# Kernel optimization log

Hardware: AMD Instinct MI355X
Metric: run time of the kernel (lower is better)

Reference implementation:

```python
import jax, jax.numpy as jnp
import numpy as np

B, E, T = 2, 512, 2048
H = 8
LOCAL_SIZE = 128
NEG_INF = -1e9


def setup_inputs() -> dict:
    key = jax.random.key(0)
    ks = jax.random.split(key, 5)
    return {
        "x": jax.random.normal(ks[0], (B, E, T), dtype=jnp.float32),
        "in_proj_w": jax.random.normal(ks[1], (3 * E, E), dtype=jnp.float32) * (E ** -0.5),
        "in_proj_b": jax.random.normal(ks[2], (3 * E,), dtype=jnp.float32) * 0.02,
        "out_w": jax.random.normal(ks[3], (E, E), dtype=jnp.float32) * (E ** -0.5),
        "out_b": jax.random.normal(ks[4], (E,), dtype=jnp.float32) * 0.02,
    }


def _local_mask(t, local_size, dtype):
    # allowed iff |i - j| <= local_size // 2 (sliding local window)
    i = jnp.arange(t)[:, None]
    j = jnp.arange(t)[None, :]
    allowed = jnp.abs(i - j) <= (local_size // 2)
    return jnp.where(allowed, jnp.zeros((), dtype), jnp.full((), NEG_INF, dtype))


def reference(x, in_proj_w, in_proj_b, out_w, out_b):
    dh = E // H
    scale = 1.0 / jnp.sqrt(jnp.asarray(dh, x.dtype))
    xt = jnp.transpose(x, (0, 2, 1))               # [B, T, E]
    qkv = xt @ in_proj_w.T + in_proj_b             # [B, T, 3E]
    q, k, v = jnp.split(qkv, 3, axis=-1)
    q = q.reshape(B, T, H, dh)
    k = k.reshape(B, T, H, dh)
    v = v.reshape(B, T, H, dh)
    scores = jnp.einsum("bqhd,bkhd->bhqk", q, k) * scale  # [B, H, T, T]
    scores = scores + _local_mask(T, LOCAL_SIZE, scores.dtype)
    attn = jax.nn.softmax(scores, axis=-1)
    ctx = jnp.einsum("bhqk,bkhd->bqhd", attn, v).reshape(B, T, E)
    attn_out = ctx @ out_w.T + out_b               # [B, T, E]
    attn_out = jnp.transpose(attn_out, (0, 2, 1))  # [B, E, T]
    return jax.nn.relu(attn_out * x)
```

## Files before the change

kernel.cpp:

```cpp
#include <hip/hip_runtime.h>
#include <stdint.h>


#define DEVI __device__ __forceinline__

typedef __attribute__((ext_vector_type(8))) short bf16x8;
typedef __attribute__((ext_vector_type(4))) float f32x4;

DEVI unsigned short f2bf(float f) {
  unsigned u = __float_as_uint(f);
  u += 0x7fffu + ((u >> 16) & 1u);
  return (unsigned short)(u >> 16);
}
DEVI float bf2f(unsigned short h) { return __uint_as_float(((unsigned)h) << 16); }

#define GLL16(gp, lp)                                                          \
  __builtin_amdgcn_global_load_lds(                                            \
      (const __attribute__((address_space(1))) void*)(gp),                     \
      (__attribute__((address_space(3))) void*)(lp), 16, 0, 0)

#define MFMA(a, b, c) __builtin_amdgcn_mfma_f32_16x16x32_bf16((a), (b), (c), 0, 0, 0)

__global__ __launch_bounds__(256) void k_prep(
    const float* __restrict__ x, const float* __restrict__ w_in,
    const float* __restrict__ w_out, unsigned short* __restrict__ xh,
    unsigned short* __restrict__ wih, unsigned short* __restrict__ woh) {
  const int tid = threadIdx.x;
  if (blockIdx.y == 16) {
    int cb = (blockIdx.z << 6) | blockIdx.x;
    const float* src;
    unsigned short* dst;
    int base;
    if (cb < 96) {
      src = w_in; dst = wih; base = cb * 8192;
    } else {
      src = w_out; dst = woh; base = (cb - 96) * 8192;
    }
#pragma unroll
    for (int k = 0; k < 8; k++) {
      int idx = base + (k * 256 + tid) * 4;
      float4 v = *(const float4*)&src[idx];
      ushort4 o;
      o.x = f2bf(v.x); o.y = f2bf(v.y); o.z = f2bf(v.z); o.w = f2bf(v.w);
      *(ushort4*)&dst[idx] = o;
    }
    return;
  }
  __shared__ float tile[32][33];
  const int b = blockIdx.z, e0 = blockIdx.y * 32, t0 = blockIdx.x * 32;
  const int j = tid & 31, i = tid >> 5;
#pragma unroll
  for (int rr = 0; rr < 4; rr++) {
    int e = e0 + i + rr * 8;
    tile[i + rr * 8][j] = x[((size_t)b * 512 + e) * 2048 + t0 + j];
  }
  __syncthreads();
#pragma unroll
  for (int rr = 0; rr < 4; rr++) {
    int t = t0 + i + rr * 8;
    float v = tile[j][i + rr * 8];
    size_t o = ((size_t)b * 2048 + t) * 512 + e0 + j;
    xh[o] = f2bf(v);
  }
}

__global__ __launch_bounds__(256) void k_gemm_qkv(
    const unsigned short* __restrict__ Ahg, const unsigned short* __restrict__ Bhg,
    const float* __restrict__ bias, unsigned short* __restrict__ Qs,
    unsigned short* __restrict__ Kks, unsigned short* __restrict__ VvT) {
  const int KD = 512;
  __shared__ __align__(16) unsigned short Ah_s[128 * 32];
  __shared__ __align__(16) unsigned short Bh_s[128 * 32];
  const int tid = threadIdx.x, lane = tid & 63, w = tid >> 6;
  const int bid = blockIdx.x;
  const int xcd = bid & 7, j5 = bid >> 3;
  const int m0 = (xcd * 4 + j5 / 12) * 128, n0 = (j5 % 12) * 128;
  const int wm = (w >> 1) * 64, wn = (w & 1) * 64;

  f32x4 acc[4][4];
#pragma unroll
  for (int i = 0; i < 4; i++)
#pragma unroll
    for (int j = 0; j < 4; j++) acc[i][j] = (f32x4){0.f, 0.f, 0.f, 0.f};

  const int srw = lane >> 2, sc = (lane & 3) * 8;
  const size_t b0 = (size_t)(n0 + w * 32 + srw) * KD + sc;
  const size_t b1 = b0 + (size_t)16 * KD;
  unsigned short* lB0 = &Bh_s[(w * 32) * 32];
  unsigned short* lB1 = &Bh_s[(w * 32 + 16) * 32];
  const size_t a0 = (size_t)(m0 + w * 32 + srw) * KD + sc;
  const size_t a1 = a0 + (size_t)16 * KD;
  unsigned short* lAh0 = &Ah_s[(w * 32) * 32];
  unsigned short* lAh1 = &Ah_s[(w * 32 + 16) * 32];

  const int fm = lane & 15, fq = (lane >> 4) * 8;

  for (int k0 = 0; k0 < KD; k0 += 32) {
    __syncthreads();
    GLL16(Ahg + a0 + k0, lAh0);
    GLL16(Ahg + a1 + k0, lAh1);
    GLL16(Bhg + b0 + k0, lB0);
    GLL16(Bhg + b1 + k0, lB1);
    __builtin_amdgcn_s_waitcnt(0);
    __syncthreads();

    bf16x8 ah[4], bh[4];
#pragma unroll
    for (int i = 0; i < 4; i++) {
      ah[i] = *(const bf16x8*)&Ah_s[(wm + i * 16 + fm) * 32 + fq];
      bh[i] = *(const bf16x8*)&Bh_s[(wn + i * 16 + fm) * 32 + fq];
    }
#pragma unroll
    for (int i = 0; i < 4; i++)
#pragma unroll
      for (int j = 0; j < 4; j++)
        acc[i][j] = MFMA(ah[i], bh[j], acc[i][j]);
  }

  const int quad = lane >> 4;
#pragma unroll
  for (int i = 0; i < 4; i++)
#pragma unroll
    for (int j = 0; j < 4; j++) {
      int gn = n0 + wn + j * 16 + fm;
      float bv = bias[gn];
      int sec = gn >> 9, cc = gn & 511;
      int h = cc >> 6, d = cc & 63;
      int gm0 = m0 + wm + i * 16 + quad * 4;
      int bb = gm0 >> 11, t = gm0 & 2047;
      if (sec == 2) {
        ushort4 pk;
        pk.x = f2bf(acc[i][j][0] + bv);
        pk.y = f2bf(acc[i][j][1] + bv);
        pk.z = f2bf(acc[i][j][2] + bv);
        pk.w = f2bf(acc[i][j][3] + bv);
        *(ushort4*)&VvT[(((size_t)(bb * 8 + h)) * 64 + d) * 2048 + t] = pk;
      } else {
        unsigned short* dst = sec == 0 ? Qs : Kks;
        float mul = sec == 0 ? 0.125f : 1.0f;
#pragma unroll
        for (int r = 0; r < 4; r++) {
          float v = (acc[i][j][r] + bv) * mul;
          dst[(((size_t)(bb * 8 + h)) * 2048 + t + r) * 64 + d] = f2bf(v);
        }
      }
    }
}

__global__ __launch_bounds__(256) void k_gemm_out(
    const unsigned short* __restrict__ Ahg, const unsigned short* __restrict__ Bhg,
    const float* __restrict__ bias, const float* __restrict__ x,
    float* __restrict__ out) {
  const int KD = 512;
  __shared__ __align__(16) union {
    struct {
      unsigned short Ah[64 * 32];
      unsigned short Bh[128 * 32];
    } st;
    float tile[64][129];
  } u;
  const int tid = threadIdx.x, lane = tid & 63, w = tid >> 6;
  const int bid = blockIdx.x;
  const int xcd = bid & 7, j5 = bid >> 3;
  const int m0 = (xcd * 8 + (j5 >> 2)) * 64, n0 = (j5 & 3) * 128;
  const int wm = (w >> 1) * 32, wn = (w & 1) * 64;

  f32x4 acc[2][4];
#pragma unroll
  for (int i = 0; i < 2; i++)
#pragma unroll
    for (int j = 0; j < 4; j++) acc[i][j] = (f32x4){0.f, 0.f, 0.f, 0.f};

  const int srw = lane >> 2, sc = (lane & 3) * 8;
  const size_t b0 = (size_t)(n0 + w * 32 + srw) * KD + sc;
  const size_t b1 = b0 + (size_t)16 * KD;
  const size_t a0 = (size_t)(m0 + w * 16 + srw) * KD + sc;
  unsigned short* lB0 = &u.st.Bh[(w * 32) * 32];
  unsigned short* lB1 = &u.st.Bh[(w * 32 + 16) * 32];
  unsigned short* lAh0 = &u.st.Ah[(w * 16) * 32];

  const int fm = lane & 15, fq = (lane >> 4) * 8;

  for (int k0 = 0; k0 < KD; k0 += 32) {
    __syncthreads();
    GLL16(Ahg + a0 + k0, lAh0);
    GLL16(Bhg + b0 + k0, lB0);
    GLL16(Bhg + b1 + k0, lB1);
    __builtin_amdgcn_s_waitcnt(0);
    __syncthreads();

    bf16x8 ah[2], bh[4];
#pragma unroll
    for (int i = 0; i < 2; i++)
      ah[i] = *(const bf16x8*)&u.st.Ah[(wm + i * 16 + fm) * 32 + fq];
#pragma unroll
    for (int j = 0; j < 4; j++)
      bh[j] = *(const bf16x8*)&u.st.Bh[(wn + j * 16 + fm) * 32 + fq];
#pragma unroll
    for (int i = 0; i < 2; i++)
#pragma unroll
      for (int j = 0; j < 4; j++)
        acc[i][j] = MFMA(ah[i], bh[j], acc[i][j]);
  }

  __syncthreads();
  const int quad = lane >> 4;
#pragma unroll
  for (int i = 0; i < 2; i++)
#pragma unroll
    for (int j = 0; j < 4; j++) {
      int ln = wn + j * 16 + fm;
      float bv = bias[n0 + ln];
#pragma unroll
      for (int r = 0; r < 4; r++) {
        int lm = wm + i * 16 + quad * 4 + r;
        u.tile[lm][ln] = acc[i][j][r] + bv;
      }
    }
  __syncthreads();

  const int bb = m0 >> 11, t0 = m0 & 2047;
  const int tt = tid & 63, e0w = tid >> 6;
#pragma unroll
  for (int k = 0; k < 32; k++) {
    int ee = e0w + k * 4;
    size_t o = ((size_t)bb * 512 + n0 + ee) * 2048 + t0 + tt;
    float v = u.tile[tt][ee] * x[o];
    out[o] = fmaxf(v, 0.f);
  }
}

#define PSTR 200
__global__ __launch_bounds__(256, 4) void k_attention(
    const unsigned short* __restrict__ Qs, const unsigned short* __restrict__ Kks,
    const unsigned short* __restrict__ VvT, unsigned short* __restrict__ ctx_hi) {
  __shared__ __align__(16) unsigned short P_s[64 * PSTR];

  const int tid = threadIdx.x, lane = tid & 63, w = tid >> 6;
  const int q0 = blockIdx.x * 64;
  const int bh = blockIdx.y;
  const int j0 = q0 - 64;
  const size_t base = (size_t)bh * 2048 * 64;
  const int fm = lane & 15, quad = lane >> 4;

  bf16x8 aq[2];
  {
    const size_t qb = base + (size_t)(q0 + w * 16 + fm) * 64 + quad * 8;
#pragma unroll
    for (int ks = 0; ks < 2; ks++)
      aq[ks] = *(const bf16x8*)&Qs[qb + ks * 32];
  }

  const int ct0 = (w >> 1) * 2;
  f32x4 sa[10];
#pragma unroll
  for (int u2 = 0; u2 < 10; u2++) sa[u2] = (f32x4){0.f, 0.f, 0.f, 0.f};
  __builtin_amdgcn_s_setprio(1);
#pragma unroll
  for (int u2 = 0; u2 < 10; u2++) {
    int jr = j0 + (ct0 + u2) * 16 + fm;
    jr = jr < 0 ? 0 : (jr > 2047 ? 2047 : jr);
    const unsigned short* kp = &Kks[base + (size_t)jr * 64 + quad * 8];
#pragma unroll
    for (int ks = 0; ks < 2; ks++) {
      bf16x8 bk = *(const bf16x8*)&kp[ks * 32];
      sa[u2] = MFMA(aq[ks], bk, sa[u2]);
    }
  }
  __builtin_amdgcn_s_setprio(0);

  float rm[4], rs[4], inv[4];
#pragma unroll
  for (int r = 0; r < 4; r++) rm[r] = -1e30f;
#pragma unroll
  for (int u2 = 0; u2 < 10; u2++) {
    int jj = (ct0 + u2) * 16 + fm;
    int jg = j0 + jj;
    bool jok = (jg >= 0) && (jg < 2048);
#pragma unroll
    for (int r = 0; r < 4; r++) {
      int ii = w * 16 + quad * 4 + r;
      bool ok = jok && (jj >= ii) && (jj <= ii + 128);
      float sv = ok ? sa[u2][r] : -1e30f;
      sa[u2][r] = sv;
      rm[r] = fmaxf(rm[r], sv);
    }
  }
#pragma unroll
  for (int off = 1; off < 16; off <<= 1)
#pragma unroll
    for (int r = 0; r < 4; r++) rm[r] = fmaxf(rm[r], __shfl_xor(rm[r], off));
#pragma unroll
  for (int r = 0; r < 4; r++) rs[r] = 0.f;
#pragma unroll
  for (int u2 = 0; u2 < 10; u2++)
#pragma unroll
    for (int r = 0; r < 4; r++) {
      float e = __expf(sa[u2][r] - rm[r]);
      sa[u2][r] = e;
      rs[r] += e;
    }
#pragma unroll
  for (int off = 1; off < 16; off <<= 1)
#pragma unroll
    for (int r = 0; r < 4; r++) rs[r] += __shfl_xor(rs[r], off);
#pragma unroll
  for (int r = 0; r < 4; r++) inv[r] = 1.0f / rs[r];

#pragma unroll
  for (int u2 = 0; u2 < 10; u2++)
#pragma unroll
    for (int r = 0; r < 4; r++) {
      int row = w * 16 + quad * 4 + r;
      P_s[row * PSTR + (ct0 + u2) * 16 + fm] = f2bf(sa[u2][r] * inv[r]);
    }
  asm volatile("s_waitcnt lgkmcnt(0)" ::: "memory");
  __builtin_amdgcn_sched_barrier(0);

  const int ks0 = w >> 1;
  f32x4 oa[4];
#pragma unroll
  for (int dt = 0; dt < 4; dt++) oa[dt] = (f32x4){0.f, 0.f, 0.f, 0.f};
  __builtin_amdgcn_s_setprio(1);
#pragma unroll
  for (int ku = 0; ku < 5; ku++) {
    int ks = ks0 + ku;
    bf16x8 ap = *(const bf16x8*)&P_s[(w * 16 + fm) * PSTR + ks * 32 + quad * 8];
    int j = j0 + ks * 32 + quad * 8;
    j = (j < 0 || j > 2040) ? 0 : j;
    const unsigned short* vp = &VvT[base + j];
#pragma unroll
    for (int dt = 0; dt < 4; dt++) {
      bf16x8 bv = *(const bf16x8*)&vp[(size_t)(dt * 16 + fm) * 2048];
      oa[dt] = MFMA(ap, bv, oa[dt]);
    }
  }
  __builtin_amdgcn_s_setprio(0);

  const int bb = bh >> 3, h = bh & 7;
#pragma unroll
  for (int dt = 0; dt < 4; dt++)
#pragma unroll
    for (int r = 0; r < 4; r++) {
      int t = q0 + w * 16 + quad * 4 + r;
      int c = h * 64 + dt * 16 + fm;
      ctx_hi[((size_t)(bb * 2048 + t)) * 512 + c] = f2bf(oa[dt][r]);
    }
}

extern "C" void kernel_launch(void* const* d_in, const int* in_sizes, int n_in,
                              void* d_out, int out_size, void* d_ws, size_t ws_size,
                              hipStream_t stream) {
  const float* x = (const float*)d_in[0];
  const float* w_in = (const float*)d_in[1];
  const float* b_in = (const float*)d_in[2];
  const float* w_out = (const float*)d_in[3];
  const float* b_out = (const float*)d_in[4];
  float* out = (float*)d_out;

  uint8_t* ws = (uint8_t*)d_ws;
  unsigned short* xT_hi = (unsigned short*)(ws + 0);
  unsigned short* wih   = (unsigned short*)(ws + 8388608);
  unsigned short* woh   = (unsigned short*)(ws + 9961472);
  unsigned short* Qs    = (unsigned short*)(ws + 12582912);
  unsigned short* Kk    = (unsigned short*)(ws + 16777216);
  unsigned short* VvT   = (unsigned short*)(ws + 20971520);
  unsigned short* ctxh  = (unsigned short*)(ws + 25165824);

  k_prep<<<dim3(64, 17, 2), 256, 0, stream>>>(x, w_in, w_out, xT_hi, wih, woh);
  k_gemm_qkv<<<384, 256, 0, stream>>>(xT_hi, wih, b_in, Qs, Kk, VvT);
  k_attention<<<dim3(32, 16), 256, 0, stream>>>(Qs, Kk, VvT, ctxh);
  k_gemm_out<<<256, 256, 0, stream>>>(ctxh, woh, b_out, x, out);
}
```

Measured before the change: 115.2 us.

## Retile prep transpose and both GEMMs with 64-wide K steps and more blocks

The prep kernel now transposes x in 64x64 tiles with float4 loads and ushort4 stores, and converts weights in larger chunks. The QKV GEMM moves to 128x96 tiles (512 blocks), and the output GEMM moves to 64x64 tiles (512 blocks). Both GEMMs now load K in steps of 64, which halves the number of barrier-separated load rounds. The aim is better occupancy across CUs, wider memory transactions and fewer syncs, at the cost of less reuse per tile and more LDS per block.

```diff
diff --git a/kernel.cpp b/kernel.cpp
--- a/kernel.cpp
+++ b/kernel.cpp
@@ -26,18 +26,18 @@
     const float* __restrict__ w_out, unsigned short* __restrict__ xh,
     unsigned short* __restrict__ wih, unsigned short* __restrict__ woh) {
   const int tid = threadIdx.x;
-  if (blockIdx.y == 16) {
-    int cb = (blockIdx.z << 6) | blockIdx.x;
+  if (blockIdx.y == 8) {
+    int cb = (blockIdx.z << 5) | blockIdx.x;
     const float* src;
     unsigned short* dst;
     int base;
-    if (cb < 96) {
-      src = w_in; dst = wih; base = cb * 8192;
+    if (cb < 48) {
+      src = w_in; dst = wih; base = cb * 16384;
     } else {
-      src = w_out; dst = woh; base = (cb - 96) * 8192;
-    }
-#pragma unroll
-    for (int k = 0; k < 8; k++) {
+      src = w_out; dst = woh; base = (cb - 48) * 16384;
+    }
+#pragma unroll
+    for (int k = 0; k < 16; k++) {
       int idx = base + (k * 256 + tid) * 4;
       float4 v = *(const float4*)&src[idx];
       ushort4 o;
@@ -46,21 +46,26 @@
     }
     return;
   }
-  __shared__ float tile[32][33];
-  const int b = blockIdx.z, e0 = blockIdx.y * 32, t0 = blockIdx.x * 32;
-  const int j = tid & 31, i = tid >> 5;
-#pragma unroll
-  for (int rr = 0; rr < 4; rr++) {
-    int e = e0 + i + rr * 8;
-    tile[i + rr * 8][j] = x[((size_t)b * 512 + e) * 2048 + t0 + j];
+  __shared__ float tile[64][65];
+  const int b = blockIdx.z, e0 = blockIdx.y * 64, t0 = blockIdx.x * 64;
+  const int g = tid >> 4, c4 = (tid & 15) * 4;
+#pragma unroll
+  for (int p = 0; p < 4; p++) {
+    int el = p * 16 + g;
+    float4 v = *(const float4*)&x[((size_t)b * 512 + e0 + el) * 2048 + t0 + c4];
+    tile[el][c4 + 0] = v.x; tile[el][c4 + 1] = v.y;
+    tile[el][c4 + 2] = v.z; tile[el][c4 + 3] = v.w;
   }
   __syncthreads();
 #pragma unroll
-  for (int rr = 0; rr < 4; rr++) {
-    int t = t0 + i + rr * 8;
-    float v = tile[j][i + rr * 8];
-    size_t o = ((size_t)b * 2048 + t) * 512 + e0 + j;
-    xh[o] = f2bf(v);
+  for (int p = 0; p < 4; p++) {
+    int tl = p * 16 + g;
+    ushort4 o;
+    o.x = f2bf(tile[c4 + 0][tl]);
+    o.y = f2bf(tile[c4 + 1][tl]);
+    o.z = f2bf(tile[c4 + 2][tl]);
+    o.w = f2bf(tile[c4 + 3][tl]);
+    *(ushort4*)&xh[((size_t)(b * 2048 + t0 + tl)) * 512 + e0 + c4] = o;
   }
 }
 
@@ -69,59 +74,61 @@
     const float* __restrict__ bias, unsigned short* __restrict__ Qs,
     unsigned short* __restrict__ Kks, unsigned short* __restrict__ VvT) {
   const int KD = 512;
-  __shared__ __align__(16) unsigned short Ah_s[128 * 32];
-  __shared__ __align__(16) unsigned short Bh_s[128 * 32];
+  __shared__ __align__(16) unsigned short Ah_s[128 * 64];
+  __shared__ __align__(16) unsigned short Bh_s[96 * 64];
   const int tid = threadIdx.x, lane = tid & 63, w = tid >> 6;
   const int bid = blockIdx.x;
   const int xcd = bid & 7, j5 = bid >> 3;
-  const int m0 = (xcd * 4 + j5 / 12) * 128, n0 = (j5 % 12) * 128;
-  const int wm = (w >> 1) * 64, wn = (w & 1) * 64;
-
-  f32x4 acc[4][4];
+  const int m0 = (xcd * 4 + (j5 >> 4)) * 128;
+  const int n0 = (j5 & 15) * 96;
+  const int wm = (w >> 1) * 64, wn = (w & 1) * 48;
+
+  f32x4 acc[4][3];
 #pragma unroll
   for (int i = 0; i < 4; i++)
 #pragma unroll
-    for (int j = 0; j < 4; j++) acc[i][j] = (f32x4){0.f, 0.f, 0.f, 0.f};
-
-  const int srw = lane >> 2, sc = (lane & 3) * 8;
-  const size_t b0 = (size_t)(n0 + w * 32 + srw) * KD + sc;
-  const size_t b1 = b0 + (size_t)16 * KD;
-  unsigned short* lB0 = &Bh_s[(w * 32) * 32];
-  unsigned short* lB1 = &Bh_s[(w * 32 + 16) * 32];
-  const size_t a0 = (size_t)(m0 + w * 32 + srw) * KD + sc;
-  const size_t a1 = a0 + (size_t)16 * KD;
-  unsigned short* lAh0 = &Ah_s[(w * 32) * 32];
-  unsigned short* lAh1 = &Ah_s[(w * 32 + 16) * 32];
-
+    for (int j = 0; j < 3; j++) acc[i][j] = (f32x4){0.f, 0.f, 0.f, 0.f};
+
+  const int srw = lane >> 3, sc = (lane & 7) * 8;
   const int fm = lane & 15, fq = (lane >> 4) * 8;
 
-  for (int k0 = 0; k0 < KD; k0 += 32) {
+  for (int k0 = 0; k0 < KD; k0 += 64) {
     __syncthreads();
-    GLL16(Ahg + a0 + k0, lAh0);
-    GLL16(Ahg + a1 + k0, lAh1);
-    GLL16(Bhg + b0 + k0, lB0);
-    GLL16(Bhg + b1 + k0, lB1);
+#pragma unroll
+    for (int ci = 0; ci < 7; ci++) {
+      int c = w + ci * 4;
+      if (c < 16) {
+        GLL16(Ahg + (size_t)(m0 + c * 8 + srw) * KD + k0 + sc, &Ah_s[c * 512]);
+      } else {
+        int cb = c - 16;
+        GLL16(Bhg + (size_t)(n0 + cb * 8 + srw) * KD + k0 + sc, &Bh_s[cb * 512]);
+      }
+    }
     __builtin_amdgcn_s_waitcnt(0);
     __syncthreads();
 
-    bf16x8 ah[4], bh[4];
-#pragma unroll
-    for (int i = 0; i < 4; i++) {
-      ah[i] = *(const bf16x8*)&Ah_s[(wm + i * 16 + fm) * 32 + fq];
-      bh[i] = *(const bf16x8*)&Bh_s[(wn + i * 16 + fm) * 32 + fq];
-    }
-#pragma unroll
-    for (int i = 0; i < 4; i++)
-#pragma unroll
-      for (int j = 0; j < 4; j++)
-        acc[i][j] = MFMA(ah[i], bh[j], acc[i][j]);
+#pragma unroll
+    for (int kk = 0; kk < 2; kk++) {
+      bf16x8 ah[4], bh[3];
+#pragma unroll
+      for (int i = 0; i < 4; i++)
+        ah[i] = *(const bf16x8*)&Ah_s[(wm + i * 16 + fm) * 64 + kk * 32 + fq];
+#pragma unroll
+      for (int j = 0; j < 3; j++)
+        bh[j] = *(const bf16x8*)&Bh_s[(wn + j * 16 + fm) * 64 + kk * 32 + fq];
+#pragma unroll
+      for (int i = 0; i < 4; i++)
+#pragma unroll
+        for (int j = 0; j < 3; j++)
+          acc[i][j] = MFMA(ah[i], bh[j], acc[i][j]);
+    }
   }
 
   const int quad = lane >> 4;
 #pragma unroll
   for (int i = 0; i < 4; i++)
 #pragma unroll
-    for (int j = 0; j < 4; j++) {
+    for (int j = 0; j < 3; j++) {
       int gn = n0 + wn + j * 16 + fm;
       float bv = bias[gn];
       int sec = gn >> 9, cc = gn & 511;
@@ -154,53 +161,57 @@
   const int KD = 512;
   __shared__ __align__(16) union {
     struct {
-      unsigned short Ah[64 * 32];
-      unsigned short Bh[128 * 32];
+      unsigned short Ah[64 * 64];
+      unsigned short Bh[64 * 64];
     } st;
-    float tile[64][129];
+    float tile[64][65];
   } u;
   const int tid = threadIdx.x, lane = tid & 63, w = tid >> 6;
   const int bid = blockIdx.x;
   const int xcd = bid & 7, j5 = bid >> 3;
-  const int m0 = (xcd * 8 + (j5 >> 2)) * 64, n0 = (j5 & 3) * 128;
-  const int wm = (w >> 1) * 32, wn = (w & 1) * 64;
-
-  f32x4 acc[2][4];
+  const int m0 = (xcd * 8 + (j5 >> 3)) * 64;
+  const int n0 = (j5 & 7) * 64;
+  const int wm = (w >> 1) * 32, wn = (w & 1) * 32;
+
+  f32x4 acc[2][2];
 #pragma unroll
   for (int i = 0; i < 2; i++)
 #pragma unroll
-    for (int j = 0; j < 4; j++) acc[i][j] = (f32x4){0.f, 0.f, 0.f, 0.f};
-
-  const int srw = lane >> 2, sc = (lane & 3) * 8;
-  const size_t b0 = (size_t)(n0 + w * 32 + srw) * KD + sc;
-  const size_t b1 = b0 + (size_t)16 * KD;
-  const size_t a0 = (size_t)(m0 + w * 16 + srw) * KD + sc;
-  unsigned short* lB0 = &u.st.Bh[(w * 32) * 32];
-  unsigned short* lB1 = &u.st.Bh[(w * 32 + 16) * 32];
-  unsigned short* lAh0 = &u.st.Ah[(w * 16) * 32];
-
+    for (int j = 0; j < 2; j++) acc[i][j] = (f32x4){0.f, 0.f, 0.f, 0.f};
+
+  const int srw = lane >> 3, sc = (lane & 7) * 8;
   const int fm = lane & 15, fq = (lane >> 4) * 8;
 
-  for (int k0 = 0; k0 < KD; k0 += 32) {
+  for (int k0 = 0; k0 < KD; k0 += 64) {
     __syncthreads();
-    GLL16(Ahg + a0 + k0, lAh0);
-    GLL16(Bhg + b0 + k0, lB0);
-    GLL16(Bhg + b1 + k0, lB1);
+#pragma unroll
+    for (int ci = 0; ci < 4; ci++) {
+      int c = w + ci * 4;
+      if (c < 8) {
+        GLL16(Ahg + (size_t)(m0 + c * 8 + srw) * KD + k0 + sc, &u.st.Ah[c * 512]);
+      } else {
+        int cb = c - 8;
+        GLL16(Bhg + (size_t)(n0 + cb * 8 + srw) * KD + k0 + sc, &u.st.Bh[cb * 512]);
+      }
+    }
     __builtin_amdgcn_s_waitcnt(0);
     __syncthreads();
 
-    bf16x8 ah[2], bh[4];
-#pragma unroll
-    for (int i = 0; i < 2; i++)
-      ah[i] = *(const bf16x8*)&u.st.Ah[(wm + i * 16 + fm) * 32 + fq];
-#pragma unroll
-    for (int j = 0; j < 4; j++)
-      bh[j] = *(const bf16x8*)&u.st.Bh[(wn + j * 16 + fm) * 32 + fq];
-#pragma unroll
-    for (int i = 0; i < 2; i++)
-#pragma unroll
-      for (int j = 0; j < 4; j++)
-        acc[i][j] = MFMA(ah[i], bh[j], acc[i][j]);
+#pragma unroll
+    for (int kk = 0; kk < 2; kk++) {
+      bf16x8 ah[2], bh[2];
+#pragma unroll
+      for (int i = 0; i < 2; i++)
+        ah[i] = *(const bf16x8*)&u.st.Ah[(wm + i * 16 + fm) * 64 + kk * 32 + fq];
+#pragma unroll
+      for (int j = 0; j < 2; j++)
+        bh[j] = *(const bf16x8*)&u.st.Bh[(wn + j * 16 + fm) * 64 + kk * 32 + fq];
+#pragma unroll
+      for (int i = 0; i < 2; i++)
+#pragma unroll
+        for (int j = 0; j < 2; j++)
+          acc[i][j] = MFMA(ah[i], bh[j], acc[i][j]);
+    }
   }
 
   __syncthreads();
@@ -208,7 +219,7 @@
 #pragma unroll
   for (int i = 0; i < 2; i++)
 #pragma unroll
-    for (int j = 0; j < 4; j++) {
+    for (int j = 0; j < 2; j++) {
       int ln = wn + j * 16 + fm;
       float bv = bias[n0 + ln];
 #pragma unroll
@@ -222,7 +233,7 @@
   const int bb = m0 >> 11, t0 = m0 & 2047;
   const int tt = tid & 63, e0w = tid >> 6;
 #pragma unroll
-  for (int k = 0; k < 32; k++) {
+  for (int k = 0; k < 16; k++) {
     int ee = e0w + k * 4;
     size_t o = ((size_t)bb * 512 + n0 + ee) * 2048 + t0 + tt;
     float v = u.tile[tt][ee] * x[o];
@@ -367,8 +378,8 @@
   unsigned short* VvT   = (unsigned short*)(ws + 20971520);
   unsigned short* ctxh  = (unsigned short*)(ws + 25165824);
 
-  k_prep<<<dim3(64, 17, 2), 256, 0, stream>>>(x, w_in, w_out, xT_hi, wih, woh);
-  k_gemm_qkv<<<384, 256, 0, stream>>>(xT_hi, wih, b_in, Qs, Kk, VvT);
+  k_prep<<<dim3(32, 9, 2), 256, 0, stream>>>(x, w_in, w_out, xT_hi, wih, woh);
+  k_gemm_qkv<<<512, 256, 0, stream>>>(xT_hi, wih, b_in, Qs, Kk, VvT);
   k_attention<<<dim3(32, 16), 256, 0, stream>>>(Qs, Kk, VvT, ctxh);
-  k_gemm_out<<<256, 256, 0, stream>>>(ctxh, woh, b_out, x, out);
-}
+  k_gemm_out<<<512, 256, 0, stream>>>(ctxh, woh, b_out, x, out);
+}
```

New measurement: 120.5 us. +4.6%, slower.
